# Performance work log

Measured on AMD Instinct MI355X. Metric: run time of the kernel, lower is better.

## Reference

```python
import jax, jax.numpy as jnp
import numpy as np

HID, NL, DSTATE, DCONV, EXPAND = 256, 2, 64, 4, 2
DIN = EXPAND * HID            # 512
NHEADS = DIN // 64            # 8 heads, headdim 64
HEADP = DIN // NHEADS         # 64
CONVDIM = DIN + 2 * DSTATE    # 640
PROJDIM = 2 * DIN + 2 * DSTATE + NHEADS  # 1160
B, T, NB = 2, 192, 62


def _rmsnorm(x, w, eps=1e-6):
    return x * jax.lax.rsqrt(jnp.mean(x * x, -1, keepdims=True) + eps) * w


def _causal_conv(x, w, b):
    # x (B,L,C), depthwise causal conv, w (C,K), b (C,)
    K = w.shape[1]
    L = x.shape[1]
    xp = jnp.pad(x, ((0, 0), (K - 1, 0), (0, 0)))
    y = b
    for k in range(K):
        y = y + xp[:, k:k + L, :] * w[:, k]
    return y


def _ssd(xh, dt, A, Bm, Cm):
    # quadratic (attention-like) form of the Mamba2 selective scan
    # xh (b,l,h,p), dt (b,l,h), A (h,), Bm/Cm (b,l,n)
    cum = jnp.cumsum(dt * A, axis=1)                    # (b,l,h)
    diff = cum[:, :, None, :] - cum[:, None, :, :]      # (b,l,s,h), <=0 for s<=l
    mask = jnp.tril(jnp.ones((xh.shape[1], xh.shape[1]), bool))
    decay = jnp.where(mask[None, :, :, None], jnp.exp(diff), 0.0)
    scores = jnp.einsum('bln,bsn->bls', Cm, Bm)[..., None] * decay * dt[:, None, :, :]
    return jnp.einsum('blsh,bshp->blhp', scores, xh)


def _mamba2(x, Win, Wconv, bconv, dt_bias, A_log, D, gn_w, Wout):
    b, l, _ = x.shape
    zxbcdt = x @ Win                                    # (b,l,PROJDIM)
    z = zxbcdt[..., :DIN]
    xBC = jax.nn.silu(_causal_conv(zxbcdt[..., DIN:DIN + CONVDIM], Wconv, bconv))
    xh = xBC[..., :DIN].reshape(b, l, NHEADS, HEADP)
    Bm = xBC[..., DIN:DIN + DSTATE]
    Cm = xBC[..., DIN + DSTATE:]
    dt = jax.nn.softplus(zxbcdt[..., -NHEADS:] + dt_bias)
    A = -jnp.exp(A_log)
    rev = lambda t: t[:, ::-1]
    y = _ssd(xh, dt, A, Bm, Cm) + rev(_ssd(rev(xh), rev(dt), A, rev(Bm), rev(Cm)))
    y = y + D[None, None, :, None] * xh
    y = _rmsnorm(y.reshape(b, l, DIN) * jax.nn.silu(z), gn_w)
    return y @ Wout


def _forward(x, tp, bp):
    batch, T_, NB_, H_ = x.shape
    for i in range(NL):
        # time axis: sequences of length T over batch*num_bands
        xt = jnp.transpose(x, (0, 2, 1, 3)).reshape(batch * NB_, T_, H_)
        xt = xt + _mamba2(_rmsnorm(xt, tp[0][i]), *(p[i] for p in tp[1:]))
        x = jnp.transpose(xt.reshape(batch, NB_, T_, H_), (0, 2, 1, 3))
        # band axis: sequences of length NB over batch*time
        xb = x.reshape(batch * T_, NB_, H_)
        xb = xb + _mamba2(_rmsnorm(xb, bp[0][i]), *(p[i] for p in bp[1:]))
        x = xb.reshape(batch, T_, NB_, H_)
    return x


def setup_inputs() -> dict:
    key = jax.random.key(0)
    ks = jax.random.split(key, 3)
    inp = {"x": jax.random.normal(ks[0], (B, T, NB, HID), jnp.float32)}
    for i, ax in enumerate(("t", "b")):
        kk = jax.random.split(ks[1 + i], 5)
        inp[ax + "_norm_w"] = jnp.ones((NL, HID), jnp.float32)
        inp[ax + "_Win"] = jax.random.normal(kk[0], (NL, HID, PROJDIM), jnp.float32) * HID ** -0.5
        inp[ax + "_Wconv"] = jax.random.normal(kk[1], (NL, CONVDIM, DCONV), jnp.float32) * DCONV ** -0.5
        inp[ax + "_bconv"] = jnp.zeros((NL, CONVDIM), jnp.float32)
        dt = jnp.exp(jax.random.uniform(kk[2], (NL, NHEADS)) * (np.log(0.1) - np.log(0.001)) + np.log(0.001))
        inp[ax + "_dt_bias"] = jnp.log(jnp.expm1(dt)).astype(jnp.float32)
        inp[ax + "_A_log"] = jnp.log(jax.random.uniform(kk[3], (NL, NHEADS), minval=1.0, maxval=16.0)).astype(jnp.float32)
        inp[ax + "_D"] = jnp.ones((NL, NHEADS), jnp.float32)
        inp[ax + "_gn_w"] = jnp.ones((NL, DIN), jnp.float32)
        inp[ax + "_Wout"] = jax.random.normal(kk[4], (NL, DIN, HID), jnp.float32) * DIN ** -0.5
    return inp


def reference(x, t_norm_w, t_Win, t_Wconv, t_bconv, t_dt_bias, t_A_log, t_D, t_gn_w, t_Wout,
              b_norm_w, b_Win, b_Wconv, b_bconv, b_dt_bias, b_A_log, b_D, b_gn_w, b_Wout):
    tp = (t_norm_w, t_Win, t_Wconv, t_bconv, t_dt_bias, t_A_log, t_D, t_gn_w, t_Wout)
    bp = (b_norm_w, b_Win, b_Wconv, b_bconv, b_dt_bias, b_A_log, b_D, b_gn_w, b_Wout)
    return _forward(x, tp, bp)
```

## Files before the change

### kernel.cpp

```cpp
#include <hip/hip_runtime.h>
#include <hip/hip_bf16.h>


#define MTOK   23808
#define PROJP  1280

typedef __attribute__((ext_vector_type(8))) short short8v;
typedef __attribute__((ext_vector_type(4))) short short4v;
typedef __attribute__((ext_vector_type(4))) float f32x4;

__device__ __forceinline__ float wave_sum64(float v) {
#pragma unroll
  for (int off = 32; off; off >>= 1) v += __shfl_xor(v, off, 64);
  return v;
}

__device__ __forceinline__ short f2bf(float f) {
  union { float f; unsigned u; } v; v.f = f;
  unsigned r = (v.u + 0x7fffu + ((v.u >> 16) & 1u)) >> 16;
  return (short)r;
}
__device__ __forceinline__ float bf2f(short s) {
  union { unsigned u; float f; } v; v.u = ((unsigned)(unsigned short)s) << 16; return v.f;
}

__device__ __forceinline__ long t_base(int m) {
  int seq = m / 192, tt = m - seq * 192;
  int b = seq / 62, nb = seq - b * 62;
  return ((long)((b * 192 + tt) * 62 + nb)) * 256;
}

__global__ __launch_bounds__(256) void k_wt(const float* __restrict__ tW,
                                            const float* __restrict__ bW,
                                            short* __restrict__ dst, int K, int N, int NP) {
  int z = blockIdx.z;
  const float* src = (z >> 1 ? bW : tW) + (long)(z & 1) * K * N;
  short* d = dst + (long)z * NP * K;
  int idx = blockIdx.x * 256 + threadIdx.x;
  if (idx >= NP * K) return;
  int n = idx / K, k = idx - n * K;
  d[idx] = (n < N) ? f2bf(src[(long)k * N + n]) : (short)0;
}

template <bool TPATH>
__global__ __launch_bounds__(256) void k_rmsnorm_in(const float* __restrict__ xio,
                                                    const float* __restrict__ w,
                                                    short* __restrict__ outb) {
  int m = blockIdx.x * 4 + (threadIdx.x >> 6);
  int lane = threadIdx.x & 63;
  long base = TPATH ? t_base(m) : (long)m * 256;
  float4 v = *(const float4*)(xio + base + lane * 4);
  float ss = v.x * v.x + v.y * v.y + v.z * v.z + v.w * v.w;
  ss = wave_sum64(ss);
  float sc = rsqrtf(ss * (1.f / 256.f) + 1e-6f);
  float4 wv = *(const float4*)(w + lane * 4);
  short4v o;
  o[0] = f2bf(v.x * sc * wv.x); o[1] = f2bf(v.y * sc * wv.y);
  o[2] = f2bf(v.z * sc * wv.z); o[3] = f2bf(v.w * sc * wv.w);
  *(short4v*)(outb + (long)m * 256 + lane * 4) = o;
}

template <int EPI>
__global__ __launch_bounds__(256) void gemm_mfma(const short* __restrict__ A,
                                                 const short* __restrict__ WT,
                                                 float* __restrict__ C,
                                                 int K, int ldc) {
  int w = threadIdx.x >> 6, lane = threadIdx.x & 63;
  int m0 = blockIdx.y * 128 + (w >> 1) * 64;
  int n0 = blockIdx.x * 128 + (w & 1) * 64;
  int lr = lane & 15, lg = lane >> 4;
  f32x4 acc[4][4];
#pragma unroll
  for (int i = 0; i < 4; ++i)
#pragma unroll
    for (int j = 0; j < 4; ++j) acc[i][j] = (f32x4){0.f, 0.f, 0.f, 0.f};
  const short* Ap = A + (long)(m0 + lr) * K + lg * 8;
  const short* Bp = WT + (long)(n0 + lr) * K + lg * 8;
#pragma unroll 2
  for (int k0 = 0; k0 < K; k0 += 32) {
    short8v a[4], b[4];
#pragma unroll
    for (int f = 0; f < 4; ++f) {
      a[f] = *(const short8v*)(Ap + (long)f * 16 * K + k0);
      b[f] = *(const short8v*)(Bp + (long)f * 16 * K + k0);
    }
#pragma unroll
    for (int i = 0; i < 4; ++i)
#pragma unroll
      for (int j = 0; j < 4; ++j)
        acc[i][j] = __builtin_amdgcn_mfma_f32_16x16x32_bf16(a[i], b[j], acc[i][j], 0, 0, 0);
  }
#pragma unroll
  for (int i = 0; i < 4; ++i)
#pragma unroll
    for (int j = 0; j < 4; ++j)
#pragma unroll
      for (int r = 0; r < 4; ++r) {
        int m = m0 + i * 16 + lg * 4 + r;
        int n = n0 + j * 16 + lr;
        if (EPI == 0) {
          C[(long)m * ldc + n] = acc[i][j][r];
        } else {
          long base = (EPI == 1) ? t_base(m) : (long)m * 256;
          C[base + n] += acc[i][j][r];
        }
      }
}

__global__ __launch_bounds__(256) void k_conv(const float* __restrict__ zx,
                                              const float* __restrict__ Wc,
                                              const float* __restrict__ bc,
                                              short* __restrict__ xBC, int L) {
  int idx = blockIdx.x * 256 + threadIdx.x;
  if (idx >= MTOK * 640) return;
  int m = idx / 640, c = idx - m * 640;
  int tpos = m % L;
  float acc = bc[c];
#pragma unroll
  for (int k = 0; k < 4; ++k) {
    int tt = tpos - 3 + k;
    if (tt >= 0) acc += Wc[c * 4 + k] * zx[(long)(m - 3 + k) * PROJP + 512 + c];
  }
  xBC[(long)m * 640 + c] = f2bf(acc / (1.f + __expf(-acc)));
}

__global__ __launch_bounds__(256) void k_scan(const float* __restrict__ zx,
                                              const float* __restrict__ dtbias,
                                              const float* __restrict__ A_log,
                                              float* __restrict__ dtb,
                                              float* __restrict__ cumb,
                                              int nseq, int L) {
  int wid = blockIdx.x * 4 + (threadIdx.x >> 6);
  if (wid >= nseq * 8) return;
  int seq = wid >> 3, h = wid & 7, lane = threadIdx.x & 63;
  float Ah = -__expf(A_log[h]);
  float bias = dtbias[h];
  float run = 0.f;
  for (int t0 = 0; t0 < L; t0 += 64) {
    int tt = t0 + lane;
    float d = 0.f;
    if (tt < L) {
      float v = zx[((long)seq * L + tt) * PROJP + 1152 + h] + bias;
      d = (v > 20.f) ? v : log1pf(__expf(v));
    }
    float s = d * Ah;
#pragma unroll
    for (int off = 1; off < 64; off <<= 1) {
      float o = __shfl_up(s, off, 64);
      if (lane >= off) s += o;
    }
    if (tt < L) {
      long m = (long)seq * L + tt;
      dtb[m * 8 + h] = d;
      cumb[m * 8 + h] = run + s;
    }
    run += __shfl(s, 63, 64);
  }
}

template <int L>
__global__ __launch_bounds__(256) void k_xt(const short* __restrict__ xbc,
                                            short* __restrict__ xT) {
  constexpr int LP = (L + 63) & ~63;
  int seq = blockIdx.x, h = blockIdx.y, st = blockIdx.z;
  __shared__ short tile[64][72];
  int t = threadIdx.x;
  for (int e = t; e < 512; e += 256) {
    int s = e >> 3, p8 = (e & 7) * 8;
    int sg = st * 64 + s;
    union { short8v v; short a[8]; } u;
    if (sg < L) u.v = *(const short8v*)(xbc + ((long)seq * L + sg) * 640 + h * 64 + p8);
    else {
#pragma unroll
      for (int j = 0; j < 8; ++j) u.a[j] = 0;
    }
    *(short8v*)&tile[s][p8] = u.v;
  }
  __syncthreads();
  for (int e = t; e < 512; e += 256) {
    int p = e >> 3, s8 = (e & 7) * 8;
    union { short8v v; short a[8]; } u;
#pragma unroll
    for (int j = 0; j < 8; ++j) u.a[j] = tile[s8 + j][p];
    *(short8v*)(xT + ((long)(seq * 8 + h) * 64 + p) * LP + st * 64 + s8) = u.v;
  }
}

template <int L, int NCH>
__global__ __launch_bounds__(256) void k_ssd4(const short* __restrict__ xbc,
                                              const short* __restrict__ xT,
                                              const float* __restrict__ dtb,
                                              const float* __restrict__ cumb,
                                              const float* __restrict__ A_log,
                                              short* __restrict__ y) {
  constexpr int LP = (L + 63) & ~63;
  constexpr bool FULL = (L % 64) == 0;
  int hg = blockIdx.x, lt = blockIdx.y, seq = blockIdx.z;
  int tid = threadIdx.x, w = tid >> 6, lane = tid & 63;
  int lr = lane & 15, lg = lane >> 4;
  int h = hg * 4 + w;
  int l0 = lt * 64;

  __shared__ float s_cb[64 * 64];
  __shared__ float s_cums[64][8];
  __shared__ float s_dts[64][8];

  float Ah = -__expf(A_log[h]);

  float cl[4], cpl[4];
#pragma unroll
  for (int i = 0; i < 4; ++i) {
    int lgl = l0 + i * 16 + lr;
    int lc = FULL ? lgl : (lgl < L ? lgl : L - 1);
    long m = (long)seq * L + lc;
    float cv = cumb[m * 8 + h];
    cl[i] = cv; cpl[i] = cv - dtb[m * 8 + h] * Ah;
  }

  f32x4 yacc[4][4];
#pragma unroll
  for (int i = 0; i < 4; ++i)
#pragma unroll
    for (int j = 0; j < 4; ++j) yacc[i][j] = (f32x4){0.f, 0.f, 0.f, 0.f};

  int crow = l0 + w * 16 + lr;
  if (!FULL) crow = crow < L ? crow : L - 1;
  const short* Cp = xbc + ((long)seq * L + crow) * 640 + 576 + lg * 8;

  for (int c = 0; c < NCH; ++c) {
    int c64 = c * 64;

    if (tid < 128) {
      int r = tid & 63;
      int sg = c64 + r;
      int sc = FULL ? sg : (sg < L ? sg : L - 1);
      const float* src = (tid < 64 ? cumb : dtb) + ((long)seq * L + sc) * 8;
      float4 v0 = *(const float4*)(src);
      float4 v1 = *(const float4*)(src + 4);
      float* dstp = (tid < 64 ? &s_cums[r][0] : &s_dts[r][0]);
      *(float4*)dstp = v0;
      *(float4*)(dstp + 4) = v1;
    }

    f32x4 cb4[4];
#pragma unroll
    for (int j = 0; j < 4; ++j) cb4[j] = (f32x4){0.f, 0.f, 0.f, 0.f};
#pragma unroll
    for (int ks = 0; ks < 2; ++ks) {
      short8v a = *(const short8v*)(Cp + ks * 32);
#pragma unroll
      for (int j = 0; j < 4; ++j) {
        int srow = c64 + j * 16 + lr;
        if (!FULL) srow = srow < L ? srow : L - 1;
        short8v b = *(const short8v*)(xbc + ((long)seq * L + srow) * 640 + 512 + lg * 8 + ks * 32);
        cb4[j] = __builtin_amdgcn_mfma_f32_16x16x32_bf16(a, b, cb4[j], 0, 0, 0);
      }
    }
#pragma unroll
    for (int j = 0; j < 4; ++j)
#pragma unroll
      for (int r = 0; r < 4; ++r) {
        int lloc = w * 16 + lg * 4 + r;
        int sloc = j * 16 + lr;
        s_cb[lloc * 64 + (sloc ^ ((lloc & 7) << 2))] = cb4[j][r];
      }

    short8v bx[2][4];
#pragma unroll
    for (int ks = 0; ks < 2; ++ks)
#pragma unroll
      for (int j = 0; j < 4; ++j)
        bx[ks][j] = *(const short8v*)(xT + ((long)(seq * 8 + h) * 64 + j * 16 + lr) * LP +
                                      c64 + ks * 32 + lg * 8);

    __syncthreads();

#pragma unroll
    for (int ks = 0; ks < 2; ++ks) {
      int sbase = ks * 32 + lg * 8;
      float cs[8], cps[8], dss[8];
#pragma unroll
      for (int e = 0; e < 8; ++e) {
        int sl = sbase + e;
        float cv = s_cums[sl][h];
        float dv = s_dts[sl][h];
        cs[e] = cv; cps[e] = cv - dv * Ah; dss[e] = dv;
      }
#pragma unroll
      for (int i = 0; i < 4; ++i) {
        int R = i * 16 + lr;
        int lgl = l0 + R;
        int sw = (R & 7) << 2;
        int c0 = sbase ^ sw;
        const float* cbrow = &s_cb[R * 64];
        f32x4 lo = *(const f32x4*)(cbrow + c0);
        f32x4 hi = *(const f32x4*)(cbrow + (c0 ^ 4));
        short8v a;
#pragma unroll
        for (int e = 0; e < 8; ++e) {
          int sgl = c64 + sbase + e;
          float cbv = (e < 4) ? lo[e & 3] : hi[e & 3];
          float wgt = 0.f;
          if (sgl <= lgl) wgt += __expf(cl[i] - cs[e]);
          if (sgl >= lgl) wgt += __expf(cps[e] - cpl[i]);
          if (!FULL && (lgl >= L || sgl >= L)) wgt = 0.f;
          a[e] = f2bf(cbv * wgt * dss[e]);
        }
#pragma unroll
        for (int j = 0; j < 4; ++j)
          yacc[i][j] = __builtin_amdgcn_mfma_f32_16x16x32_bf16(a, bx[ks][j], yacc[i][j], 0, 0, 0);
      }
    }
    if (c + 1 < NCH) __syncthreads();
  }

#pragma unroll
  for (int i = 0; i < 4; ++i)
#pragma unroll
    for (int r = 0; r < 4; ++r) {
      int lgl = l0 + i * 16 + lg * 4 + r;
      if (FULL || lgl < L) {
        short* yp = y + ((long)seq * L + lgl) * 512 + h * 64 + lr;
#pragma unroll
        for (int j = 0; j < 4; ++j) yp[j * 16] = f2bf(yacc[i][j][r]);
      }
    }
}

__global__ __launch_bounds__(256) void k_gate2(const short* __restrict__ y,
                                               const float* __restrict__ zx,
                                               const short* __restrict__ xbc,
                                               const float* __restrict__ Dp,
                                               const float* __restrict__ gnw,
                                               short* __restrict__ ybh) {
  int m = blockIdx.x * 4 + (threadIdx.x >> 6);
  int lane = threadIdx.x & 63;
  int d0 = lane * 8;
  short8v yv = *(const short8v*)(y + (long)m * 512 + d0);
  short8v xv = *(const short8v*)(xbc + (long)m * 640 + d0);
  float4 za = *(const float4*)(zx + (long)m * PROJP + d0);
  float4 zb = *(const float4*)(zx + (long)m * PROJP + d0 + 4);
  float Dh = Dp[lane >> 3];
  float zf[8] = {za.x, za.y, za.z, za.w, zb.x, zb.y, zb.z, zb.w};
  float g[8];
  float ss = 0.f;
#pragma unroll
  for (int i = 0; i < 8; ++i) {
    float zi = zf[i];
    g[i] = (bf2f(yv[i]) + Dh * bf2f(xv[i])) * zi / (1.f + __expf(-zi));
    ss += g[i] * g[i];
  }
  ss = wave_sum64(ss);
  float scl = rsqrtf(ss * (1.f / 512.f) + 1e-6f);
  short8v o;
#pragma unroll
  for (int i = 0; i < 8; ++i) o[i] = f2bf(g[i] * scl * gnw[d0 + i]);
  *(short8v*)(ybh + (long)m * 512 + d0) = o;
}

extern "C" void kernel_launch(void* const* d_in, const int* in_sizes, int n_in,
                              void* d_out, int out_size, void* d_ws, size_t ws_size,
                              hipStream_t stream) {
  (void)in_sizes; (void)n_in; (void)out_size; (void)ws_size;
  const float* x = (const float*)d_in[0];
  float* out = (float*)d_out;
  const long M = MTOK;

  char* p = (char*)d_ws;
  float* zx = (float*)p;     p += (size_t)M * PROJP * 4;
  short* bufn = (short*)p;   p += (size_t)M * 256 * 2;
  short* xbc = (short*)p;    p += (size_t)M * 640 * 2 + 4096;
  float* dtb = (float*)p;    p += (size_t)M * 8 * 4;
  float* cumb = (float*)p;   p += (size_t)M * 8 * 4;
  short* ybuf = (short*)p;   p += (size_t)M * 512 * 2;
  short* xT = (short*)p;     p += (size_t)12582912 * 2;
  short* ybh = (short*)p;    p += (size_t)M * 512 * 2;
  short* WinT = (short*)p;   p += (size_t)4 * PROJP * 256 * 2;
  short* WoutT = (short*)p;  p += (size_t)4 * 256 * 512 * 2;

  k_wt<<<dim3((PROJP * 256 + 255) / 256, 1, 4), 256, 0, stream>>>(
      (const float*)d_in[2], (const float*)d_in[11], WinT, 256, 1160, PROJP);
  k_wt<<<dim3((256 * 512 + 255) / 256, 1, 4), 256, 0, stream>>>(
      (const float*)d_in[9], (const float*)d_in[18], WoutT, 512, 256, 256);

  hipMemcpyAsync(out, x, (size_t)M * 256 * sizeof(float), hipMemcpyDeviceToDevice, stream);

  for (int layer = 0; layer < 2; ++layer) {
    for (int path = 0; path < 2; ++path) {
      const float* const* P = (const float* const*)(d_in + 1 + path * 9);
      const float* nw = P[0] + layer * 256;
      const float* Wc = P[2] + layer * 640 * 4;
      const float* bc = P[3] + layer * 640;
      const float* dtbias = P[4] + layer * 8;
      const float* Alog = P[5] + layer * 8;
      const float* Dp = P[6] + layer * 8;
      const float* gnw = P[7] + layer * 512;
      const short* WinTp = WinT + (long)(path * 2 + layer) * PROJP * 256;
      const short* WoutTp = WoutT + (long)(path * 2 + layer) * 256 * 512;
      int L = (path == 0) ? 192 : 62;
      int nseq = (path == 0) ? 124 : 384;

      if (path == 0) k_rmsnorm_in<true><<<MTOK / 4, 256, 0, stream>>>(out, nw, bufn);
      else           k_rmsnorm_in<false><<<MTOK / 4, 256, 0, stream>>>(out, nw, bufn);

      gemm_mfma<0><<<dim3(PROJP / 128, MTOK / 128), 256, 0, stream>>>(bufn, WinTp, zx, 256, PROJP);

      k_conv<<<(MTOK * 640 + 255) / 256, 256, 0, stream>>>(zx, Wc, bc, xbc, L);
      k_scan<<<(nseq * 8 + 3) / 4, 256, 0, stream>>>(zx, dtbias, Alog, dtb, cumb, nseq, L);

      if (path == 0) k_xt<192><<<dim3(nseq, 8, 3), 256, 0, stream>>>(xbc, xT);
      else           k_xt<62><<<dim3(nseq, 8, 1), 256, 0, stream>>>(xbc, xT);

      if (path == 0) k_ssd4<192, 3><<<dim3(2, 3, nseq), 256, 0, stream>>>(xbc, xT, dtb, cumb, Alog, ybuf);
      else           k_ssd4<62, 1><<<dim3(2, 1, nseq), 256, 0, stream>>>(xbc, xT, dtb, cumb, Alog, ybuf);

      k_gate2<<<MTOK / 4, 256, 0, stream>>>(ybuf, zx, xbc, Dp, gnw, ybh);

      if (path == 0) gemm_mfma<1><<<dim3(2, MTOK / 128), 256, 0, stream>>>(ybh, WoutTp, out, 512, 0);
      else           gemm_mfma<2><<<dim3(2, MTOK / 128), 256, 0, stream>>>(ybh, WoutTp, out, 512, 0);
    }
  }
}
```

Baseline: 1.135 ms.

## Store in-projection as bf16 with separate fp32 dt, vectorize conv

The in-projection GEMM now writes the z/xBC part of its output as bf16 in a 1152-wide buffer and writes the 8 dt columns separately in fp32. This halves the large intermediate's write and read traffic. The depthwise conv now processes 8 channels per thread with vector loads, and the GEMM remaps workgroup IDs across XCDs to improve L2 locality. Storing z and the conv inputs in bf16 lowers their precision.

```diff
diff --git a/kernel.cpp b/kernel.cpp
--- a/kernel.cpp
+++ b/kernel.cpp
@@ -4,6 +4,7 @@
 
 #define MTOK   23808
 #define PROJP  1280
+#define ZXW    1152
 
 typedef __attribute__((ext_vector_type(8))) short short8v;
 typedef __attribute__((ext_vector_type(4))) short short4v;
@@ -60,6 +61,62 @@
   *(short4v*)(outb + (long)m * 256 + lane * 4) = o;
 }
 
+__global__ __launch_bounds__(256) void gemm_in(const short* __restrict__ A,
+                                               const short* __restrict__ WT,
+                                               short* __restrict__ zxh,
+                                               float* __restrict__ dtraw) {
+  int bid = blockIdx.y * 10 + blockIdx.x;
+  int xcd = bid & 7, idx = bid >> 3;
+  const int q = 232, r = 4;
+  int wg = (xcd < r ? xcd * (q + 1) : r * (q + 1) + (xcd - r) * q) + idx;
+  int bx = wg % 10, by = wg / 10;
+
+  int w = threadIdx.x >> 6, lane = threadIdx.x & 63;
+  int m0 = by * 128 + (w >> 1) * 64;
+  int n0 = bx * 128 + (w & 1) * 64;
+  int lr = lane & 15, lg = lane >> 4;
+  f32x4 acc[4][4];
+#pragma unroll
+  for (int i = 0; i < 4; ++i)
+#pragma unroll
+    for (int j = 0; j < 4; ++j) acc[i][j] = (f32x4){0.f, 0.f, 0.f, 0.f};
+  const short* Ap = A + (long)(m0 + lr) * 256 + lg * 8;
+  const short* Bp = WT + (long)(n0 + lr) * 256 + lg * 8;
+#pragma unroll 2
+  for (int k0 = 0; k0 < 256; k0 += 32) {
+    short8v a[4], b[4];
+#pragma unroll
+    for (int f = 0; f < 4; ++f) {
+      a[f] = *(const short8v*)(Ap + (long)f * 16 * 256 + k0);
+      b[f] = *(const short8v*)(Bp + (long)f * 16 * 256 + k0);
+    }
+#pragma unroll
+    for (int i = 0; i < 4; ++i)
+#pragma unroll
+      for (int j = 0; j < 4; ++j)
+        acc[i][j] = __builtin_amdgcn_mfma_f32_16x16x32_bf16(a[i], b[j], acc[i][j], 0, 0, 0);
+  }
+  if (n0 < ZXW) {
+#pragma unroll
+    for (int i = 0; i < 4; ++i)
+#pragma unroll
+      for (int j = 0; j < 4; ++j)
+#pragma unroll
+        for (int rr = 0; rr < 4; ++rr) {
+          int m = m0 + i * 16 + lg * 4 + rr;
+          zxh[(long)m * ZXW + n0 + j * 16 + lr] = f2bf(acc[i][j][rr]);
+        }
+  } else if (n0 == ZXW && lr < 8) {
+#pragma unroll
+    for (int i = 0; i < 4; ++i)
+#pragma unroll
+      for (int rr = 0; rr < 4; ++rr) {
+        int m = m0 + i * 16 + lg * 4 + rr;
+        dtraw[(long)m * 8 + lr] = acc[i][0][rr];
+      }
+  }
+}
+
 template <int EPI>
 __global__ __launch_bounds__(256) void gemm_mfma(const short* __restrict__ A,
                                                  const short* __restrict__ WT,
@@ -95,36 +152,50 @@
 #pragma unroll
     for (int j = 0; j < 4; ++j)
 #pragma unroll
-      for (int r = 0; r < 4; ++r) {
-        int m = m0 + i * 16 + lg * 4 + r;
+      for (int rr = 0; rr < 4; ++rr) {
+        int m = m0 + i * 16 + lg * 4 + rr;
         int n = n0 + j * 16 + lr;
-        if (EPI == 0) {
-          C[(long)m * ldc + n] = acc[i][j][r];
-        } else {
-          long base = (EPI == 1) ? t_base(m) : (long)m * 256;
-          C[base + n] += acc[i][j][r];
-        }
-      }
-}
-
-__global__ __launch_bounds__(256) void k_conv(const float* __restrict__ zx,
+        long base = (EPI == 1) ? t_base(m) : (long)m * 256;
+        C[base + n] += acc[i][j][rr];
+      }
+}
+
+__global__ __launch_bounds__(256) void k_conv(const short* __restrict__ zin,
                                               const float* __restrict__ Wc,
                                               const float* __restrict__ bc,
                                               short* __restrict__ xBC, int L) {
   int idx = blockIdx.x * 256 + threadIdx.x;
-  if (idx >= MTOK * 640) return;
-  int m = idx / 640, c = idx - m * 640;
+  if (idx >= MTOK * 80) return;
+  int m = idx / 80, c8 = (idx - m * 80) << 3;
   int tpos = m % L;
-  float acc = bc[c];
+  float wv[8][4];
+#pragma unroll
+  for (int e = 0; e < 8; ++e) {
+    float4 we = *(const float4*)(Wc + (c8 + e) * 4);
+    wv[e][0] = we.x; wv[e][1] = we.y; wv[e][2] = we.z; wv[e][3] = we.w;
+  }
+  float acc[8];
+  float4 b0 = *(const float4*)(bc + c8);
+  float4 b1 = *(const float4*)(bc + c8 + 4);
+  acc[0] = b0.x; acc[1] = b0.y; acc[2] = b0.z; acc[3] = b0.w;
+  acc[4] = b1.x; acc[5] = b1.y; acc[6] = b1.z; acc[7] = b1.w;
+  const short* base = zin + (long)m * ZXW + 512 + c8;
 #pragma unroll
   for (int k = 0; k < 4; ++k) {
     int tt = tpos - 3 + k;
-    if (tt >= 0) acc += Wc[c * 4 + k] * zx[(long)(m - 3 + k) * PROJP + 512 + c];
-  }
-  xBC[(long)m * 640 + c] = f2bf(acc / (1.f + __expf(-acc)));
-}
-
-__global__ __launch_bounds__(256) void k_scan(const float* __restrict__ zx,
+    if (tt >= 0) {
+      short8v v = *(const short8v*)(base + (long)(k - 3) * ZXW);
+#pragma unroll
+      for (int e = 0; e < 8; ++e) acc[e] += wv[e][k] * bf2f(v[e]);
+    }
+  }
+  short8v o;
+#pragma unroll
+  for (int e = 0; e < 8; ++e) o[e] = f2bf(acc[e] / (1.f + __expf(-acc[e])));
+  *(short8v*)(xBC + (long)m * 640 + c8) = o;
+}
+
+__global__ __launch_bounds__(256) void k_scan(const float* __restrict__ dtraw,
                                               const float* __restrict__ dtbias,
                                               const float* __restrict__ A_log,
                                               float* __restrict__ dtb,
@@ -140,7 +211,7 @@
     int tt = t0 + lane;
     float d = 0.f;
     if (tt < L) {
-      float v = zx[((long)seq * L + tt) * PROJP + 1152 + h] + bias;
+      float v = dtraw[((long)seq * L + tt) * 8 + h] + bias;
       d = (v > 20.f) ? v : log1pf(__expf(v));
     }
     float s = d * Ah;
@@ -231,13 +302,13 @@
     int c64 = c * 64;
 
     if (tid < 128) {
-      int r = tid & 63;
-      int sg = c64 + r;
+      int rr = tid & 63;
+      int sg = c64 + rr;
       int sc = FULL ? sg : (sg < L ? sg : L - 1);
       const float* src = (tid < 64 ? cumb : dtb) + ((long)seq * L + sc) * 8;
       float4 v0 = *(const float4*)(src);
       float4 v1 = *(const float4*)(src + 4);
-      float* dstp = (tid < 64 ? &s_cums[r][0] : &s_dts[r][0]);
+      float* dstp = (tid < 64 ? &s_cums[rr][0] : &s_dts[rr][0]);
       *(float4*)dstp = v0;
       *(float4*)(dstp + 4) = v1;
     }
@@ -259,10 +330,10 @@
 #pragma unroll
     for (int j = 0; j < 4; ++j)
 #pragma unroll
-      for (int r = 0; r < 4; ++r) {
-        int lloc = w * 16 + lg * 4 + r;
+      for (int rr = 0; rr < 4; ++rr) {
+        int lloc = w * 16 + lg * 4 + rr;
         int sloc = j * 16 + lr;
-        s_cb[lloc * 64 + (sloc ^ ((lloc & 7) << 2))] = cb4[j][r];
+        s_cb[lloc * 64 + (sloc ^ ((lloc & 7) << 2))] = cb4[j][rr];
       }
 
     short8v bx[2][4];
@@ -317,18 +388,18 @@
 #pragma unroll
   for (int i = 0; i < 4; ++i)
 #pragma unroll
-    for (int r = 0; r < 4; ++r) {
-      int lgl = l0 + i * 16 + lg * 4 + r;
+    for (int rr = 0; rr < 4; ++rr) {
+      int lgl = l0 + i * 16 + lg * 4 + rr;
       if (FULL || lgl < L) {
         short* yp = y + ((long)seq * L + lgl) * 512 + h * 64 + lr;
 #pragma unroll
-        for (int j = 0; j < 4; ++j) yp[j * 16] = f2bf(yacc[i][j][r]);
+        for (int j = 0; j < 4; ++j) yp[j * 16] = f2bf(yacc[i][j][rr]);
       }
     }
 }
 
 __global__ __launch_bounds__(256) void k_gate2(const short* __restrict__ y,
-                                               const float* __restrict__ zx,
+                                               const short* __restrict__ zxh,
                                                const short* __restrict__ xbc,
                                                const float* __restrict__ Dp,
                                                const float* __restrict__ gnw,
@@ -338,15 +409,13 @@
   int d0 = lane * 8;
   short8v yv = *(const short8v*)(y + (long)m * 512 + d0);
   short8v xv = *(const short8v*)(xbc + (long)m * 640 + d0);
-  float4 za = *(const float4*)(zx + (long)m * PROJP + d0);
-  float4 zb = *(const float4*)(zx + (long)m * PROJP + d0 + 4);
+  short8v zv = *(const short8v*)(zxh + (long)m * ZXW + d0);
   float Dh = Dp[lane >> 3];
-  float zf[8] = {za.x, za.y, za.z, za.w, zb.x, zb.y, zb.z, zb.w};
   float g[8];
   float ss = 0.f;
 #pragma unroll
   for (int i = 0; i < 8; ++i) {
-    float zi = zf[i];
+    float zi = bf2f(zv[i]);
     g[i] = (bf2f(yv[i]) + Dh * bf2f(xv[i])) * zi / (1.f + __expf(-zi));
     ss += g[i] * g[i];
   }
@@ -367,7 +436,8 @@
   const long M = MTOK;
 
   char* p = (char*)d_ws;
-  float* zx = (float*)p;     p += (size_t)M * PROJP * 4;
+  short* zxh = (short*)p;    p += (size_t)M * ZXW * 2;
+  float* dtraw = (float*)p;  p += (size_t)M * 8 * 4;
   short* bufn = (short*)p;   p += (size_t)M * 256 * 2;
   short* xbc = (short*)p;    p += (size_t)M * 640 * 2 + 4096;
   float* dtb = (float*)p;    p += (size_t)M * 8 * 4;
@@ -403,10 +473,10 @@
       if (path == 0) k_rmsnorm_in<true><<<MTOK / 4, 256, 0, stream>>>(out, nw, bufn);
       else           k_rmsnorm_in<false><<<MTOK / 4, 256, 0, stream>>>(out, nw, bufn);
 
-      gemm_mfma<0><<<dim3(PROJP / 128, MTOK / 128), 256, 0, stream>>>(bufn, WinTp, zx, 256, PROJP);
-
-      k_conv<<<(MTOK * 640 + 255) / 256, 256, 0, stream>>>(zx, Wc, bc, xbc, L);
-      k_scan<<<(nseq * 8 + 3) / 4, 256, 0, stream>>>(zx, dtbias, Alog, dtb, cumb, nseq, L);
+      gemm_in<<<dim3(10, MTOK / 128), 256, 0, stream>>>(bufn, WinTp, zxh, dtraw);
+
+      k_conv<<<(MTOK * 80 + 255) / 256, 256, 0, stream>>>(zxh, Wc, bc, xbc, L);
+      k_scan<<<(nseq * 8 + 3) / 4, 256, 0, stream>>>(dtraw, dtbias, Alog, dtb, cumb, nseq, L);
 
       if (path == 0) k_xt<192><<<dim3(nseq, 8, 3), 256, 0, stream>>>(xbc, xT);
       else           k_xt<62><<<dim3(nseq, 8, 1), 256, 0, stream>>>(xbc, xT);
@@ -414,7 +484,7 @@
       if (path == 0) k_ssd4<192, 3><<<dim3(2, 3, nseq), 256, 0, stream>>>(xbc, xT, dtb, cumb, Alog, ybuf);
       else           k_ssd4<62, 1><<<dim3(2, 1, nseq), 256, 0, stream>>>(xbc, xT, dtb, cumb, Alog, ybuf);
 
-      k_gate2<<<MTOK / 4, 256, 0, stream>>>(ybuf, zx, xbc, Dp, gnw, ybh);
+      k_gate2<<<MTOK / 4, 256, 0, stream>>>(ybuf, zxh, xbc, Dp, gnw, ybh);
 
       if (path == 0) gemm_mfma<1><<<dim3(2, MTOK / 128), 256, 0, stream>>>(ybh, WoutTp, out, 512, 0);
       else           gemm_mfma<2><<<dim3(2, MTOK / 128), 256, 0, stream>>>(ybh, WoutTp, out, 512, 0);
```

Measured after the change: 1.060 ms. 1.07x faster.
